# Optimization experiments

Hardware: AMD Instinct MI355X
Metric: run time of the kernel (lower is better)

## Reference

```python
import jax, jax.numpy as jnp
import numpy as np

EPS = 1e-05
KERNEL_SIZE = 9
KERNEL_VOL = float(KERNEL_SIZE ** 3)

_DN = ("NDHWC", "DHWIO", "NDHWC")


def _box_sum(x, k=KERNEL_SIZE):
    """Sliding-window sum over a k^3 box with SAME zero padding.

    The TF module uses a dense all-ones (k,k,k) conv3d; an all-ones kernel is
    separable, so three 1D passes compute the identical result with O(k) work.
    x: (B, D1, D2, D3, 1) float.
    """
    for kshape in ((k, 1, 1), (1, k, 1), (1, 1, k)):
        w = jnp.ones(kshape + (1, 1), dtype=x.dtype)
        x = jax.lax.conv_general_dilated(
            x, w, window_strides=(1, 1, 1), padding="SAME",
            dimension_numbers=_DN)
    return x


def setup_inputs() -> dict:
    key = jax.random.key(0)
    k1, k2 = jax.random.split(key)
    shape = (2, 192, 192, 192)
    y_true = jax.random.uniform(k1, shape, dtype=jnp.float32)
    y_pred = jax.random.uniform(k2, shape, dtype=jnp.float32)
    return {"y_true": y_true, "y_pred": y_pred}


def reference(y_true, y_pred):
    # Expand (B, D1, D2, D3) -> (B, D1, D2, D3, 1) as in the TF call().
    if y_true.ndim == 4:
        y_true = y_true[..., None]
        y_pred = y_pred[..., None]

    t_sum = _box_sum(y_true)
    p_sum = _box_sum(y_pred)
    tp_sum = _box_sum(y_true * y_pred)

    t_avg = t_sum / KERNEL_VOL
    p_avg = p_sum / KERNEL_VOL

    cross = tp_sum - p_avg * t_sum
    num = cross * cross + EPS  # the DEBUG1 variant returns `num` directly
    return num
```

## Files before the change

### kernel.cpp

```cpp
#include <hip/hip_runtime.h>


#define N 192
#define RSTRIDE 46

#define LDS_BARRIER() asm volatile("s_waitcnt lgkmcnt(0)\n\ts_barrier" ::: "memory")

__global__ __launch_bounds__(1024, 4)
void lncc_kernel(const float* __restrict__ t_in,
                 const float* __restrict__ p_in,
                 float* __restrict__ out)
{
    __shared__ __align__(16) float rowT[3 * 32 * RSTRIDE];
    __shared__ float pcol[3 * 32 * 32];

    const int bid = blockIdx.x;
    int xy, Z, z0;
    if (bid < 64) {
        xy = bid >> 3;
        Z  = 24;
        z0 = (bid & 7) * 24;
    } else {
        const int q  = bid - 64;
        xy = 8 + q / 7;
        const int zi = q % 7;
        if (zi < 3) { Z = 28; z0 = zi * 28; }
        else        { Z = 27; z0 = 84 + (zi - 3) * 27; }
    }
    const int b  = xy / 36;
    const int t6 = xy % 36;
    const int y0 = (t6 / 6) * 32, x0 = (t6 % 6) * 32;
    const int tid = threadIdx.x;

    const int  lf   = tid / 320;
    const int  ls   = tid - lf * 320;
    const int  lry  = ls >> 3;
    const int  lxq  = ls & 7;
    const int  lgy  = y0 - 4 + lry;
    const int  lgx0 = x0 - 4 + 4 * lxq;
    const bool lactive = (tid < 960);
    const bool lyok = ((unsigned)lgy < (unsigned)N);

    const int  cf  = tid >> 8;
    const int  cyq = (tid >> 5) & 7;
    const int  cx  = tid & 31;
    const bool cactive = (tid < 768);

    const int gx = tid & 31;
    const int gy = tid >> 5;

    const size_t plane = (size_t)N * N;
    const float* tb = t_in + (size_t)b * N * plane;
    const float* pb = p_in + (size_t)b * N * plane;
    float*       ob = out  + (size_t)b * N * plane
                           + (size_t)(y0 + gy) * N + (x0 + gx);

    float ring_t[9], ring_p[9], ring_tp[9];
    float sum_t = 0.f, sum_p = 0.f, sum_tp = 0.f;
    #pragma unroll
    for (int i = 0; i < 9; ++i) { ring_t[i] = 0.f; ring_p[i] = 0.f; ring_tp[i] = 0.f; }

    const float4 z4 = make_float4(0.f, 0.f, 0.f, 0.f);
    float4 cur0 = z4, cur1 = z4, cur2 = z4;

    {
        const int zp0 = z0 - 4;
        if (((unsigned)zp0 < (unsigned)N) && lactive && lyok) {
            const float* rt = tb + (size_t)zp0 * plane + (size_t)lgy * N;
            const float* rp = pb + (size_t)zp0 * plane + (size_t)lgy * N;
            float4 a[3], c[3];
            #pragma unroll
            for (int q = 0; q < 3; ++q) {
                a[q] = z4; c[q] = z4;
                const int gxq = lgx0 + 4 * q;
                if ((unsigned)gxq < (unsigned)N) {
                    a[q] = (lf == 1) ? *(const float4*)(rp + gxq)
                                     : *(const float4*)(rt + gxq);
                    if (lf == 2) c[q] = *(const float4*)(rp + gxq);
                }
            }
            if (lf == 2) {
                #pragma unroll
                for (int q = 0; q < 3; ++q) {
                    a[q].x *= c[q].x; a[q].y *= c[q].y;
                    a[q].z *= c[q].z; a[q].w *= c[q].w;
                }
            }
            cur0 = a[0]; cur1 = a[1]; cur2 = a[2];
        }
    }

    #pragma unroll 1
    for (int k = 0; k < 4; ++k) {
      #pragma unroll
      for (int r = 0; r < 9; ++r) {
        const int i  = k * 9 + r;
        const int zp = z0 - 4 + i;
        const int zn = zp + 1;
        const bool vi = (i < Z + 8)     && ((unsigned)zp < (unsigned)N);
        const bool vn = (i + 1 < Z + 8) && ((unsigned)zn < (unsigned)N);

        float4 fa0 = z4, fa1 = z4, fa2 = z4, fc0 = z4, fc1 = z4, fc2 = z4;
        if (vn && lactive && lyok) {
            const float* rt = tb + (size_t)zn * plane + (size_t)lgy * N;
            const float* rp = pb + (size_t)zn * plane + (size_t)lgy * N;
            const int g0 = lgx0, g1 = lgx0 + 4, g2 = lgx0 + 8;
            if ((unsigned)g0 < (unsigned)N) {
                fa0 = (lf == 1) ? *(const float4*)(rp + g0) : *(const float4*)(rt + g0);
                if (lf == 2) fc0 = *(const float4*)(rp + g0);
            }
            if ((unsigned)g1 < (unsigned)N) {
                fa1 = (lf == 1) ? *(const float4*)(rp + g1) : *(const float4*)(rt + g1);
                if (lf == 2) fc1 = *(const float4*)(rp + g1);
            }
            if ((unsigned)g2 < (unsigned)N) {
                fa2 = (lf == 1) ? *(const float4*)(rp + g2) : *(const float4*)(rt + g2);
                if (lf == 2) fc2 = *(const float4*)(rp + g2);
            }
        }

        if (vi && lactive) {
            const float v0 = cur0.x, v1 = cur0.y, v2  = cur0.z, v3  = cur0.w;
            const float v4 = cur1.x, v5 = cur1.y, v6  = cur1.z, v7  = cur1.w;
            const float v8 = cur2.x, v9 = cur2.y, v10 = cur2.z, v11 = cur2.w;
            float s0 = ((v0+v1) + (v2+v3)) + ((v4+v5) + (v6+v7)) + v8;
            float s1 = s0 - v0 + v9;
            float s2 = s1 - v1 + v10;
            float s3 = s2 - v2 + v11;
            float* wp = &rowT[(lf * 32 + 4 * lxq) * RSTRIDE + lry];
            wp[0]           = s0;
            wp[RSTRIDE]     = s1;
            wp[2 * RSTRIDE] = s2;
            wp[3 * RSTRIDE] = s3;
        }
        LDS_BARRIER();

        if (vi && cactive) {
            const float* rb = &rowT[(cf * 32 + cx) * RSTRIDE + 4 * cyq];
            const float2 u0 = *(const float2*)(rb + 0);
            const float2 u1 = *(const float2*)(rb + 2);
            const float2 u2 = *(const float2*)(rb + 4);
            const float2 u3 = *(const float2*)(rb + 6);
            const float2 u4 = *(const float2*)(rb + 8);
            const float2 u5 = *(const float2*)(rb + 10);
            const float w0=u0.x, w1=u0.y, w2=u1.x,  w3=u1.y;
            const float w4=u2.x, w5=u2.y, w6=u3.x,  w7=u3.y;
            const float w8=u4.x, w9=u4.y, w10=u5.x, w11=u5.y;
            float c0 = ((w0+w1)+(w2+w3)) + ((w4+w5)+(w6+w7)) + w8;
            float c1 = c0 - w0 + w9;
            float c2 = c1 - w1 + w10;
            float c3 = c2 - w2 + w11;
            float* pc = &pcol[cf * 1024 + (4 * cyq) * 32 + cx];
            pc[0]  = c0;
            pc[32] = c1;
            pc[64] = c2;
            pc[96] = c3;
        }
        LDS_BARRIER();

        float Pt = 0.f, Pp = 0.f, Ptp = 0.f;
        if (vi) {
            Pt  = pcol[       gy * 32 + gx];
            Pp  = pcol[1024 + gy * 32 + gx];
            Ptp = pcol[2048 + gy * 32 + gx];
        }
        sum_t  += Pt  - ring_t[r];  ring_t[r]  = Pt;
        sum_p  += Pp  - ring_p[r];  ring_p[r]  = Pp;
        sum_tp += Ptp - ring_tp[r]; ring_tp[r] = Ptp;
        if (i >= 8 && i < Z + 8) {
            const float cross = sum_tp - (sum_p * (1.0f / 729.0f)) * sum_t;
            ob[(size_t)(z0 + i - 8) * plane] = cross * cross + 1e-5f;
        }

        if (vn && lactive) {
            float4 A0 = fa0, A1 = fa1, A2 = fa2;
            if (lf == 2) {
                A0.x *= fc0.x; A0.y *= fc0.y; A0.z *= fc0.z; A0.w *= fc0.w;
                A1.x *= fc1.x; A1.y *= fc1.y; A1.z *= fc1.z; A1.w *= fc1.w;
                A2.x *= fc2.x; A2.y *= fc2.y; A2.z *= fc2.z; A2.w *= fc2.w;
            }
            cur0 = A0; cur1 = A1; cur2 = A2;
        }
      }
    }
}

extern "C" void kernel_launch(void* const* d_in, const int* in_sizes, int n_in,
                              void* d_out, int out_size, void* d_ws, size_t ws_size,
                              hipStream_t stream) {
    const float* y_true = (const float*)d_in[0];
    const float* y_pred = (const float*)d_in[1];
    float* out = (float*)d_out;
    dim3 grid(512);
    dim3 block(1024);
    hipLaunchKernelGGL(lncc_kernel, grid, block, 0, stream, y_true, y_pred, out);
}
```

Before: 211.6 us.

## Software-pipeline row, column and z stages with double-buffered LDS, one barrier

```diff
diff --git a/kernel.cpp b/kernel.cpp
--- a/kernel.cpp
+++ b/kernel.cpp
@@ -3,16 +3,18 @@
 
 #define N 192
 #define RSTRIDE 46
+#define RBUF (3 * 32 * RSTRIDE)
+#define PBUF (3 * 32 * 32)
 
 #define LDS_BARRIER() asm volatile("s_waitcnt lgkmcnt(0)\n\ts_barrier" ::: "memory")
 
-__global__ __launch_bounds__(1024, 4)
+__global__ __launch_bounds__(1024, 8)
 void lncc_kernel(const float* __restrict__ t_in,
                  const float* __restrict__ p_in,
                  float* __restrict__ out)
 {
-    __shared__ __align__(16) float rowT[3 * 32 * RSTRIDE];
-    __shared__ float pcol[3 * 32 * 32];
+    __shared__ __align__(16) float rowT[2 * RBUF];
+    __shared__ __align__(16) float pcol[2 * PBUF];
 
     const int bid = blockIdx.x;
     int xy, Z, z0;
@@ -27,6 +29,8 @@
         if (zi < 3) { Z = 28; z0 = zi * 28; }
         else        { Z = 27; z0 = 84 + (zi - 3) * 27; }
     }
+    const int P = Z + 8;
+
     const int b  = xy / 36;
     const int t6 = xy % 36;
     const int y0 = (t6 / 6) * 32, x0 = (t6 % 6) * 32;
@@ -40,6 +44,10 @@
     const int  lgx0 = x0 - 4 + 4 * lxq;
     const bool lactive = (tid < 960);
     const bool lyok = ((unsigned)lgy < (unsigned)N);
+    const bool lv   = lactive && lyok;
+    const bool q0ok = ((unsigned)lgx0 < (unsigned)N);
+    const bool q1ok = ((unsigned)(lgx0 + 4) < (unsigned)N);
+    const bool q2ok = ((unsigned)(lgx0 + 8) < (unsigned)N);
 
     const int  cf  = tid >> 8;
     const int  cyq = (tid >> 5) & 7;
@@ -55,6 +63,16 @@
     float*       ob = out  + (size_t)b * N * plane
                            + (size_t)(y0 + gy) * N + (x0 + gx);
 
+    const int lgyc = lyok ? lgy : 0;
+    const float* const trow = tb + (size_t)lgyc * N;
+    const float* const prow = pb + (size_t)lgyc * N;
+    const float* const arow = (lf == 1) ? prow : trow;
+
+    float* const       wpA = &rowT[(lf * 32 + 4 * lxq) * RSTRIDE + lry];
+    const float* const rbB = &rowT[(cf * 32 + cx) * RSTRIDE + 4 * cyq];
+    float* const       pcB = &pcol[cf * 1024 + (4 * cyq) * 32 + cx];
+    const float* const pgC = &pcol[gy * 32 + gx];
+
     float ring_t[9], ring_p[9], ring_tp[9];
     float sum_t = 0.f, sum_p = 0.f, sum_tp = 0.f;
     #pragma unroll
@@ -62,127 +80,115 @@
 
     const float4 z4 = make_float4(0.f, 0.f, 0.f, 0.f);
     float4 cur0 = z4, cur1 = z4, cur2 = z4;
-
-    {
-        const int zp0 = z0 - 4;
-        if (((unsigned)zp0 < (unsigned)N) && lactive && lyok) {
-            const float* rt = tb + (size_t)zp0 * plane + (size_t)lgy * N;
-            const float* rp = pb + (size_t)zp0 * plane + (size_t)lgy * N;
-            float4 a[3], c[3];
-            #pragma unroll
-            for (int q = 0; q < 3; ++q) {
-                a[q] = z4; c[q] = z4;
-                const int gxq = lgx0 + 4 * q;
-                if ((unsigned)gxq < (unsigned)N) {
-                    a[q] = (lf == 1) ? *(const float4*)(rp + gxq)
-                                     : *(const float4*)(rt + gxq);
-                    if (lf == 2) c[q] = *(const float4*)(rp + gxq);
-                }
-            }
-            if (lf == 2) {
-                #pragma unroll
-                for (int q = 0; q < 3; ++q) {
-                    a[q].x *= c[q].x; a[q].y *= c[q].y;
-                    a[q].z *= c[q].z; a[q].w *= c[q].w;
-                }
-            }
-            cur0 = a[0]; cur1 = a[1]; cur2 = a[2];
-        }
-    }
+    float4 fa0, fa1, fa2, fc0, fc1, fc2;
+
+#define ISSUE_LOADS(ZOFS, COND) do { \
+    fa0 = z4; fa1 = z4; fa2 = z4; fc0 = z4; fc1 = z4; fc2 = z4; \
+    if (COND) { \
+        const float* ar = arow + (ZOFS); \
+        const float* cr = prow + (ZOFS); \
+        if (q0ok) { fa0 = *(const float4*)(ar + lgx0);     if (lf == 2) fc0 = *(const float4*)(cr + lgx0); } \
+        if (q1ok) { fa1 = *(const float4*)(ar + lgx0 + 4); if (lf == 2) fc1 = *(const float4*)(cr + lgx0 + 4); } \
+        if (q2ok) { fa2 = *(const float4*)(ar + lgx0 + 8); if (lf == 2) fc2 = *(const float4*)(cr + lgx0 + 8); } \
+    } } while (0)
+
+#define FINALIZE() do { \
+    if (lf == 2) { \
+        fa0.x *= fc0.x; fa0.y *= fc0.y; fa0.z *= fc0.z; fa0.w *= fc0.w; \
+        fa1.x *= fc1.x; fa1.y *= fc1.y; fa1.z *= fc1.z; fa1.w *= fc1.w; \
+        fa2.x *= fc2.x; fa2.y *= fc2.y; fa2.z *= fc2.z; fa2.w *= fc2.w; \
+    } \
+    cur0 = fa0; cur1 = fa1; cur2 = fa2; } while (0)
+
+#define ROWSUM_STORE(BOFS) do { if (lactive) { \
+    const float v0 = cur0.x, v1 = cur0.y, v2  = cur0.z, v3  = cur0.w; \
+    const float v4 = cur1.x, v5 = cur1.y, v6  = cur1.z, v7  = cur1.w; \
+    const float v8 = cur2.x, v9 = cur2.y, v10 = cur2.z, v11 = cur2.w; \
+    const float s0 = ((v0 + v1) + (v2 + v3)) + ((v4 + v5) + (v6 + v7)) + v8; \
+    const float s1 = s0 - v0 + v9; \
+    const float s2 = s1 - v1 + v10; \
+    const float s3 = s2 - v2 + v11; \
+    float* wp = wpA + (BOFS); \
+    wp[0] = s0; wp[RSTRIDE] = s1; wp[2 * RSTRIDE] = s2; wp[3 * RSTRIDE] = s3; } } while (0)
+
+#define COLSUM(ROFS, POFS) do { if (cactive) { \
+    const float* rb = rbB + (ROFS); \
+    const float2 u0 = *(const float2*)(rb + 0); \
+    const float2 u1 = *(const float2*)(rb + 2); \
+    const float2 u2 = *(const float2*)(rb + 4); \
+    const float2 u3 = *(const float2*)(rb + 6); \
+    const float2 u4 = *(const float2*)(rb + 8); \
+    const float2 u5 = *(const float2*)(rb + 10); \
+    const float w0 = u0.x, w1 = u0.y, w2  = u1.x, w3  = u1.y; \
+    const float w4 = u2.x, w5 = u2.y, w6  = u3.x, w7  = u3.y; \
+    const float w8 = u4.x, w9 = u4.y, w10 = u5.x, w11 = u5.y; \
+    const float c0 = ((w0 + w1) + (w2 + w3)) + ((w4 + w5) + (w6 + w7)) + w8; \
+    const float c1 = c0 - w0 + w9; \
+    const float c2 = c1 - w1 + w10; \
+    const float c3 = c2 - w2 + w11; \
+    float* pc = pcB + (POFS); \
+    pc[0] = c0; pc[32] = c1; pc[64] = c2; pc[96] = c3; } } while (0)
+
+    ISSUE_LOADS((long)(z0 - 4) * (long)plane,
+                ((unsigned)(z0 - 4) < (unsigned)N) && lv);
+    FINALIZE();
+    ROWSUM_STORE(0);
+    ISSUE_LOADS((long)(z0 - 3) * (long)plane,
+                ((unsigned)(z0 - 3) < (unsigned)N) && lv);
+    FINALIZE();
+    LDS_BARRIER();
+
+    long zoff = (long)(z0 - 2) * (long)plane;
 
     #pragma unroll 1
-    for (int k = 0; k < 4; ++k) {
+    for (int k = 0; k < 5; ++k) {
       #pragma unroll
       for (int r = 0; r < 9; ++r) {
-        const int i  = k * 9 + r;
-        const int zp = z0 - 4 + i;
-        const int zn = zp + 1;
-        const bool vi = (i < Z + 8)     && ((unsigned)zp < (unsigned)N);
-        const bool vn = (i + 1 < Z + 8) && ((unsigned)zn < (unsigned)N);
-
-        float4 fa0 = z4, fa1 = z4, fa2 = z4, fc0 = z4, fc1 = z4, fc2 = z4;
-        if (vn && lactive && lyok) {
-            const float* rt = tb + (size_t)zn * plane + (size_t)lgy * N;
-            const float* rp = pb + (size_t)zn * plane + (size_t)lgy * N;
-            const int g0 = lgx0, g1 = lgx0 + 4, g2 = lgx0 + 8;
-            if ((unsigned)g0 < (unsigned)N) {
-                fa0 = (lf == 1) ? *(const float4*)(rp + g0) : *(const float4*)(rt + g0);
-                if (lf == 2) fc0 = *(const float4*)(rp + g0);
-            }
-            if ((unsigned)g1 < (unsigned)N) {
-                fa1 = (lf == 1) ? *(const float4*)(rp + g1) : *(const float4*)(rt + g1);
-                if (lf == 2) fc1 = *(const float4*)(rp + g1);
-            }
-            if ((unsigned)g2 < (unsigned)N) {
-                fa2 = (lf == 1) ? *(const float4*)(rp + g2) : *(const float4*)(rt + g2);
-                if (lf == 2) fc2 = *(const float4*)(rp + g2);
-            }
+        const int j = k * 9 + r;
+        if (j > P) break;
+
+        ISSUE_LOADS(zoff,
+                    (j + 2 < P) && ((unsigned)(z0 + j - 2) < (unsigned)N) && lv);
+
+        const int pj    = j & 1;
+        const int rofsA = (pj ^ 1) * RBUF;
+        const int rofsB = pj * RBUF;
+        const int pofsB = pj * PBUF;
+        const int pofsC = (pj ^ 1) * PBUF;
+
+        ROWSUM_STORE(rofsA);
+
+        COLSUM(rofsB, pofsB);
+
+        float Pt = 0.f, Pp = 0.f, Ptp = 0.f;
+        if ((j >= 1) && ((unsigned)(z0 + j - 5) < (unsigned)N)) {
+            const float* pg = pgC + pofsC;
+            Pt  = pg[0];
+            Pp  = pg[1024];
+            Ptp = pg[2048];
         }
-
-        if (vi && lactive) {
-            const float v0 = cur0.x, v1 = cur0.y, v2  = cur0.z, v3  = cur0.w;
-            const float v4 = cur1.x, v5 = cur1.y, v6  = cur1.z, v7  = cur1.w;
-            const float v8 = cur2.x, v9 = cur2.y, v10 = cur2.z, v11 = cur2.w;
-            float s0 = ((v0+v1) + (v2+v3)) + ((v4+v5) + (v6+v7)) + v8;
-            float s1 = s0 - v0 + v9;
-            float s2 = s1 - v1 + v10;
-            float s3 = s2 - v2 + v11;
-            float* wp = &rowT[(lf * 32 + 4 * lxq) * RSTRIDE + lry];
-            wp[0]           = s0;
-            wp[RSTRIDE]     = s1;
-            wp[2 * RSTRIDE] = s2;
-            wp[3 * RSTRIDE] = s3;
+        {
+            const int s = (r + 8) % 9;
+            sum_t  += Pt  - ring_t[s];  ring_t[s]  = Pt;
+            sum_p  += Pp  - ring_p[s];  ring_p[s]  = Pp;
+            sum_tp += Ptp - ring_tp[s]; ring_tp[s] = Ptp;
         }
+        if (j >= 9) {
+            const float cross = sum_tp - (sum_p * (1.0f / 729.0f)) * sum_t;
+            ob[(size_t)(z0 + j - 9) * plane] = cross * cross + 1e-5f;
+        }
+
+        FINALIZE();
+        zoff += (long)plane;
+
         LDS_BARRIER();
-
-        if (vi && cactive) {
-            const float* rb = &rowT[(cf * 32 + cx) * RSTRIDE + 4 * cyq];
-            const float2 u0 = *(const float2*)(rb + 0);
-            const float2 u1 = *(const float2*)(rb + 2);
-            const float2 u2 = *(const float2*)(rb + 4);
-            const float2 u3 = *(const float2*)(rb + 6);
-            const float2 u4 = *(const float2*)(rb + 8);
-            const float2 u5 = *(const float2*)(rb + 10);
-            const float w0=u0.x, w1=u0.y, w2=u1.x,  w3=u1.y;
-            const float w4=u2.x, w5=u2.y, w6=u3.x,  w7=u3.y;
-            const float w8=u4.x, w9=u4.y, w10=u5.x, w11=u5.y;
-            float c0 = ((w0+w1)+(w2+w3)) + ((w4+w5)+(w6+w7)) + w8;
-            float c1 = c0 - w0 + w9;
-            float c2 = c1 - w1 + w10;
-            float c3 = c2 - w2 + w11;
-            float* pc = &pcol[cf * 1024 + (4 * cyq) * 32 + cx];
-            pc[0]  = c0;
-            pc[32] = c1;
-            pc[64] = c2;
-            pc[96] = c3;
-        }
-        LDS_BARRIER();
-
-        float Pt = 0.f, Pp = 0.f, Ptp = 0.f;
-        if (vi) {
-            Pt  = pcol[       gy * 32 + gx];
-            Pp  = pcol[1024 + gy * 32 + gx];
-            Ptp = pcol[2048 + gy * 32 + gx];
-        }
-        sum_t  += Pt  - ring_t[r];  ring_t[r]  = Pt;
-        sum_p  += Pp  - ring_p[r];  ring_p[r]  = Pp;
-        sum_tp += Ptp - ring_tp[r]; ring_tp[r] = Ptp;
-        if (i >= 8 && i < Z + 8) {
-            const float cross = sum_tp - (sum_p * (1.0f / 729.0f)) * sum_t;
-            ob[(size_t)(z0 + i - 8) * plane] = cross * cross + 1e-5f;
-        }
-
-        if (vn && lactive) {
-            float4 A0 = fa0, A1 = fa1, A2 = fa2;
-            if (lf == 2) {
-                A0.x *= fc0.x; A0.y *= fc0.y; A0.z *= fc0.z; A0.w *= fc0.w;
-                A1.x *= fc1.x; A1.y *= fc1.y; A1.z *= fc1.z; A1.w *= fc1.w;
-                A2.x *= fc2.x; A2.y *= fc2.y; A2.z *= fc2.z; A2.w *= fc2.w;
-            }
-            cur0 = A0; cur1 = A1; cur2 = A2;
-        }
       }
     }
+
+#undef ISSUE_LOADS
+#undef FINALIZE
+#undef ROWSUM_STORE
+#undef COLSUM
 }
 
 extern "C" void kernel_launch(void* const* d_in, const int* in_sizes, int n_in,
```

Result: slower. 613.6 us (+190.0%).
